# Kernel optimization log

Hardware: AMD Instinct MI355X
Metric: run time of the kernel (lower is better)

Reference implementation:

```python
import jax, jax.numpy as jnp
import numpy as np

T = 5            # Newton-Schulz iterations
NORM_GROUPS = 16 # groups along out_channels
EPS = 1e-5


def setup_inputs() -> dict:
    key = jax.random.key(0)
    # conv weight: [out_ch, in_ch, kh, kw]
    weight = jax.random.normal(key, (2048, 1024, 3, 3), dtype=jnp.float32) * 0.05
    return {"weight": weight}


def reference(weight):
    g = NORM_GROUPS
    out_ch = weight.shape[0]
    Z = weight.reshape(g, out_ch // g, -1)                 # [g, n, d]
    Zc = Z - Z.mean(axis=-1, keepdims=True)                # center each row
    S = jnp.einsum('gnd,gmd->gnm', Zc, Zc)                 # [g, n, n] covariance
    n = S.shape[-1]
    eye = jnp.eye(n, dtype=S.dtype)
    S = S + EPS * eye
    norm_S = jnp.sqrt(jnp.sum(S * S, axis=(1, 2), keepdims=True))  # fro norm, [g,1,1]
    S = S / norm_S

    B0 = jnp.broadcast_to(eye, S.shape)                    # B[0] = I

    def body(B, _):
        B3 = B @ B @ B                                     # matrix_power3
        Bn = 1.5 * B - 0.5 * (B3 @ S)                      # baddbmm(1.5, B, -0.5, B^3, S)
        return Bn, None

    Bt, _ = jax.lax.scan(body, B0, None, length=T)
    W = (Bt @ Zc) / jnp.sqrt(norm_S)                       # [g, n, d]
    return W.reshape(weight.shape)
```

## Files before the change

### kernel.cpp

```cpp
#include <hip/hip_runtime.h>


#define G 16
#define NROW 128
#define D 9216
#define OC 2048
#define KSPLIT 32
#define KCHUNK 288
#define EPSV 1e-5f

typedef float f32x16 __attribute__((ext_vector_type(16)));
typedef __bf16 bf16x8 __attribute__((ext_vector_type(8)));

union Frag {
    uint4 q;
    unsigned short s[8];
    bf16x8 v;
};

static __device__ __forceinline__ unsigned short f2bf(float x) {
    union { float f; unsigned int u; } a; a.f = x;
    unsigned int u = a.u;
    unsigned int r = u + 0x7FFFu + ((u >> 16) & 1u);
    return (unsigned short)(r >> 16);
}

static __device__ __forceinline__ float bf2f(unsigned short s) {
    union { unsigned int u; float f; } a; a.u = ((unsigned int)s) << 16;
    return a.f;
}

static __device__ __forceinline__ int swz(int r, int c) {
    return (r << 7) + ((((c >> 3) ^ (r & 15)) << 3) | (c & 7));
}

__global__ __launch_bounds__(256) void k_sgemm(const float* __restrict__ W,
                                               unsigned short* __restrict__ Zraw,
                                               float* __restrict__ Spart,
                                               float* __restrict__ rowsumPart) {
    __shared__ unsigned short tile[NROW * 128];
    __shared__ float rsum[NROW];
    int bid = blockIdx.x;
    int g = bid >> 5, ks = bid & 31;
    int t = threadIdx.x, lane = t & 63, wave = t >> 6;
    int mq = (wave & 1) * 64, nq = (wave >> 1) * 64;
    int m = lane & 31, h = lane >> 5;

    if (t < 128) rsum[t] = 0.f;

    f32x16 acc[2][2];
#pragma unroll
    for (int i = 0; i < 2; i++)
#pragma unroll
        for (int j = 0; j < 2; j++)
#pragma unroll
            for (int z = 0; z < 16; z++) acc[i][j][z] = 0.f;

    float rs[16], rq[4];
#pragma unroll
    for (int i = 0; i < 16; i++) rs[i] = 0.f;
#pragma unroll
    for (int i = 0; i < 4; i++) rq[i] = 0.f;

    const float* wg = W + (size_t)g * NROW * D + ks * KCHUNK;
    unsigned short* zo = Zraw + (size_t)g * NROW * D + ks * KCHUNK;

    float4 pf[16];
#pragma unroll
    for (int p = 0; p < 16; p++) {
        int fl = p * 256 + t, r = fl >> 5, cf = fl & 31;
        pf[p] = *(const float4*)(wg + (size_t)r * D + cf * 4);
    }

    for (int step = 0; step < 3; step++) {
        __syncthreads();
        if (step < 2) {
            int dbase = step * 128;
#pragma unroll
            for (int p = 0; p < 16; p++) {
                int fl = p * 256 + t, r = fl >> 5, cf = fl & 31;
                float4 x = pf[p];
                rs[p] += x.x + x.y + x.z + x.w;
                ushort4 pk;
                pk.x = f2bf(x.x); pk.y = f2bf(x.y);
                pk.z = f2bf(x.z); pk.w = f2bf(x.w);
                *(ushort4*)(zo + (size_t)r * D + dbase + cf * 4) = pk;
                union { ushort4 s4; uint2 u; } cv; cv.s4 = pk;
                *(uint2*)(tile + swz(r, cf * 4)) = cv.u;
            }
        } else {
#pragma unroll
            for (int p = 0; p < 4; p++) {
                int fl = p * 256 + t, r = fl >> 3, cf = fl & 7;
                float4 x = pf[p];
                rq[p] += x.x + x.y + x.z + x.w;
                ushort4 pk;
                pk.x = f2bf(x.x); pk.y = f2bf(x.y);
                pk.z = f2bf(x.z); pk.w = f2bf(x.w);
                *(ushort4*)(zo + (size_t)r * D + 256 + cf * 4) = pk;
                union { ushort4 s4; uint2 u; } cv; cv.s4 = pk;
                *(uint2*)(tile + swz(r, cf * 4)) = cv.u;
            }
        }
        __syncthreads();
        if (step == 0) {
#pragma unroll
            for (int p = 0; p < 16; p++) {
                int fl = p * 256 + t, r = fl >> 5, cf = fl & 31;
                pf[p] = *(const float4*)(wg + (size_t)r * D + 128 + cf * 4);
            }
        } else if (step == 1) {
#pragma unroll
            for (int p = 0; p < 4; p++) {
                int fl = p * 256 + t, r = fl >> 3, cf = fl & 7;
                pf[p] = *(const float4*)(wg + (size_t)r * D + 256 + cf * 4);
            }
        }
        int kmax = (step < 2) ? 8 : 2;
#pragma unroll
        for (int kk = 0; kk < 8; kk++) {
            if (kk >= kmax) break;
            int kb = kk * 16 + h * 8;
            Frag a0, a1, b0, b1;
            a0.q = *(const uint4*)(tile + swz(mq + m, kb));
            a1.q = *(const uint4*)(tile + swz(mq + 32 + m, kb));
            b0.q = *(const uint4*)(tile + swz(nq + m, kb));
            b1.q = *(const uint4*)(tile + swz(nq + 32 + m, kb));
            acc[0][0] = __builtin_amdgcn_mfma_f32_32x32x16_bf16(a0.v, b0.v, acc[0][0], 0, 0, 0);
            acc[0][1] = __builtin_amdgcn_mfma_f32_32x32x16_bf16(a0.v, b1.v, acc[0][1], 0, 0, 0);
            acc[1][0] = __builtin_amdgcn_mfma_f32_32x32x16_bf16(a1.v, b0.v, acc[1][0], 0, 0, 0);
            acc[1][1] = __builtin_amdgcn_mfma_f32_32x32x16_bf16(a1.v, b1.v, acc[1][1], 0, 0, 0);
        }
    }
    float* sp = Spart + (size_t)bid * 16384;
#pragma unroll
    for (int i = 0; i < 2; i++)
#pragma unroll
        for (int j = 0; j < 2; j++)
#pragma unroll
            for (int reg = 0; reg < 16; reg++) {
                int row = (reg & 3) + 8 * (reg >> 2) + 4 * h;
                sp[(mq + i * 32 + row) * 128 + nq + j * 32 + m] = acc[i][j][reg];
            }
#pragma unroll
    for (int p = 0; p < 16; p++) atomicAdd(&rsum[p * 8 + (t >> 5)], rs[p]);
#pragma unroll
    for (int p = 0; p < 4; p++) atomicAdd(&rsum[p * 32 + (t >> 3)], rq[p]);
    __syncthreads();
    if (t < 128) rowsumPart[bid * 128 + t] = rsum[t];
}

__global__ __launch_bounds__(256) void k_reduce(const float* __restrict__ Spart,
                                                const float* __restrict__ rowsumPart,
                                                float* __restrict__ Sred,
                                                float* __restrict__ normPart) {
    __shared__ float muv[128];
    __shared__ float ls[4];
    int b = blockIdx.x;
    int g = b >> 4, part = b & 15;
    int t = threadIdx.x;
    if (t < 128) {
        float s = 0.f;
        for (int ks = 0; ks < KSPLIT; ks++) s += rowsumPart[(g * KSPLIT + ks) * 128 + t];
        muv[t] = s * (1.0f / 9216.0f);
    }
    __syncthreads();
    int el = part * 1024 + t * 4;
    float4 s = {0.f, 0.f, 0.f, 0.f};
    for (int ks = 0; ks < KSPLIT; ks++) {
        float4 p = *(const float4*)(Spart + (size_t)(g * KSPLIT + ks) * 16384 + el);
        s.x += p.x; s.y += p.y; s.z += p.z; s.w += p.w;
    }
    int r = el >> 7, c = el & 127;
    float4 mc = *(float4*)&muv[c];
    float dm = 9216.0f * muv[r];
    s.x -= dm * mc.x; s.y -= dm * mc.y; s.z -= dm * mc.z; s.w -= dm * mc.w;
    if (r >= c && r <= c + 3) {
        if (r == c) s.x += EPSV;
        else if (r == c + 1) s.y += EPSV;
        else if (r == c + 2) s.z += EPSV;
        else s.w += EPSV;
    }
    *(float4*)(Sred + (size_t)g * 16384 + el) = s;
    float sq = s.x * s.x + s.y * s.y + s.z * s.z + s.w * s.w;
#pragma unroll
    for (int o = 32; o > 0; o >>= 1) sq += __shfl_down(sq, o, 64);
    if ((t & 63) == 0) ls[t >> 6] = sq;
    __syncthreads();
    if (t == 0) normPart[b] = ls[0] + ls[1] + ls[2] + ls[3];
}

__global__ __launch_bounds__(512) void k_ns(const float* __restrict__ Sred,
                                            const float* __restrict__ normPart,
                                            const float* __restrict__ rowsumPart,
                                            unsigned short* __restrict__ Bt,
                                            float* __restrict__ cvec) {
    extern __shared__ unsigned short sm[];
    unsigned short* Bb = sm;
    unsigned short* Sb = sm + 16384;
    unsigned short* Ub = sm + 32768;
    unsigned short* Vt = sm + 49152;
    int g = blockIdx.x;
    int t = threadIdx.x, lane = t & 63, wave = t >> 6;
    int m = lane & 31, h = lane >> 5;

    float ns = 0.f;
#pragma unroll
    for (int i = 0; i < 16; i++) ns += normPart[g * 16 + i];
    float rn = 1.0f / sqrtf(ns);

    {
        int r = t >> 2, c0 = (t & 3) * 32;
        const float* sp = Sred + (size_t)g * 16384 + r * 128 + c0;
#pragma unroll
        for (int q = 0; q < 4; q++) {
            int c = c0 + q * 8;
            float4 x0 = *(const float4*)(sp + q * 8);
            float4 x1 = *(const float4*)(sp + q * 8 + 4);
            float vv[8] = {x0.x, x0.y, x0.z, x0.w, x1.x, x1.y, x1.z, x1.w};
            Frag fs, fb;
#pragma unroll
            for (int i = 0; i < 8; i++) {
                float sv = vv[i] * rn;
                fs.s[i] = f2bf(sv);
                float bv = -0.5f * sv + ((r == c + i) ? 1.5f : 0.f);
                fb.s[i] = f2bf(bv);
            }
            *(uint4*)(Sb + swz(r, c)) = fs.q;
            *(uint4*)(Bb + swz(r, c)) = fb.q;
        }
    }
    Frag fI[2];
#pragma unroll
    for (int kk2 = 0; kk2 < 2; kk2++)
#pragma unroll
        for (int j = 0; j < 8; j++)
            fI[kk2].s[j] = (m == kk2 * 16 + h * 8 + j) ? (unsigned short)0x3FC0
                                                       : (unsigned short)0;
    __syncthreads();

    for (int iter = 0; iter < 4; iter++) {
#pragma unroll
        for (int i = 0; i < 4; i++) {
            int task = wave * 4 + i;
            int tmb = ((task >> 2) & 3) * 32, tnb = (task & 3) * 32;
            const unsigned short* Bsrc = (task < 16) ? Bb : Sb;
            unsigned short* dst = (task < 16) ? Ub : Vt;
            float sc = (task < 16) ? 1.0f : -0.5f;
            f32x16 acc;
#pragma unroll
            for (int z = 0; z < 16; z++) acc[z] = 0.f;
#pragma unroll
            for (int kk = 0; kk < 8; kk++) {
                Frag a, bfr;
                a.q = *(const uint4*)(Bb + swz(tmb + m, kk * 16 + h * 8));
                bfr.q = *(const uint4*)(Bsrc + swz(tnb + m, kk * 16 + h * 8));
                acc = __builtin_amdgcn_mfma_f32_32x32x16_bf16(a.v, bfr.v, acc, 0, 0, 0);
            }
#pragma unroll
            for (int q = 0; q < 4; q++) {
                union { unsigned short s[4]; uint2 u; } pk;
#pragma unroll
                for (int j = 0; j < 4; j++) pk.s[j] = f2bf(sc * acc[q * 4 + j]);
                *(uint2*)(dst + swz(tnb + m, tmb + q * 8 + h * 4)) = pk.u;
            }
        }
        __syncthreads();
        f32x16 acc2[2];
#pragma unroll
        for (int i = 0; i < 2; i++) {
            int task = wave * 2 + i;
            int tmb = (task >> 2) * 32, tnb = (task & 3) * 32;
#pragma unroll
            for (int z = 0; z < 16; z++) acc2[i][z] = 0.f;
#pragma unroll
            for (int kk = 0; kk < 8; kk++) {
                Frag a, bfr;
                a.q = *(const uint4*)(Ub + swz(tmb + m, kk * 16 + h * 8));
                bfr.q = *(const uint4*)(Vt + swz(tnb + m, kk * 16 + h * 8));
                acc2[i] = __builtin_amdgcn_mfma_f32_32x32x16_bf16(a.v, bfr.v, acc2[i], 0, 0, 0);
            }
#pragma unroll
            for (int kk2 = 0; kk2 < 2; kk2++) {
                Frag bfr;
                bfr.q = *(const uint4*)(Bb + swz(tnb + m, tmb + kk2 * 16 + h * 8));
                acc2[i] = __builtin_amdgcn_mfma_f32_32x32x16_bf16(fI[kk2].v, bfr.v, acc2[i], 0, 0, 0);
            }
        }
        __syncthreads();
#pragma unroll
        for (int i = 0; i < 2; i++) {
            int task = wave * 2 + i;
            int tmb = (task >> 2) * 32, tnb = (task & 3) * 32;
#pragma unroll
            for (int q = 0; q < 4; q++) {
                union { unsigned short s[4]; uint2 u; } pk;
#pragma unroll
                for (int j = 0; j < 4; j++) pk.s[j] = f2bf(acc2[i][q * 4 + j]);
                *(uint2*)(Bb + swz(tnb + m, tmb + q * 8 + h * 4)) = pk.u;
            }
        }
        __syncthreads();
    }
    {
        int r = t >> 2, c0 = (t & 3) * 32;
        unsigned short* bp = Bt + (size_t)g * 16384 + r * 128;
#pragma unroll
        for (int q = 0; q < 4; q++) {
            uint4 dd = *(const uint4*)(Bb + swz(r, c0 + q * 8));
            *(uint4*)(bp + c0 + q * 8) = dd;
        }
    }
    float* muv = (float*)(sm + 32768);
    if (t < 128) {
        float s = 0.f;
        for (int ks = 0; ks < KSPLIT; ks++) s += rowsumPart[(g * KSPLIT + ks) * 128 + t];
        muv[t] = s * (1.0f / 9216.0f);
    }
    __syncthreads();
    if (t < 128) {
        float cacc = 0.f;
        for (int k = 0; k < 128; k++) cacc += bf2f(Bb[swz(t, k)]) * muv[k];
        cvec[g * 128 + t] = cacc;
    }
}

__global__ __launch_bounds__(256) void k_wgemm(const unsigned short* __restrict__ Zraw,
                                               const unsigned short* __restrict__ Bt,
                                               const float* __restrict__ normPart,
                                               const float* __restrict__ cvec,
                                               float* __restrict__ out) {
    __shared__ unsigned short Ab[16384];
    __shared__ unsigned short Zt[16384];
    __shared__ float cs[128];
    int nt = blockIdx.x, g = blockIdx.y;
    int t = threadIdx.x, lane = t & 63, wave = t >> 6;
    int m = lane & 31, h = lane >> 5;

    float nsum = 0.f;
#pragma unroll
    for (int i = 0; i < 16; i++) nsum += normPart[g * 16 + i];
    float ss = 1.0f / sqrtf(sqrtf(nsum));

    const unsigned short* bg = Bt + (size_t)g * 16384;
    const unsigned short* zg = Zraw + (size_t)g * NROW * D + nt * 128;
#pragma unroll
    for (int p = 0; p < 8; p++) {
        int flat = p * 256 + t;
        int r = flat >> 4, gc = flat & 15;
        uint4 da = *(const uint4*)(bg + r * 128 + gc * 8);
        uint4 dz = *(const uint4*)(zg + (size_t)r * D + gc * 8);
        *(uint4*)(Ab + swz(r, gc * 8)) = da;
        *(uint4*)(Zt + swz(r, gc * 8)) = dz;
    }
    if (t < 128) cs[t] = cvec[g * 128 + t] * ss;
    __syncthreads();

    int cw = wave * 32 + m;

    f32x16 acc[4];
#pragma unroll
    for (int i = 0; i < 4; i++)
#pragma unroll
        for (int z = 0; z < 16; z++) acc[i][z] = 0.f;

#pragma unroll
    for (int ks = 0; ks < 8; ks++) {
        int k0 = ks * 16 + h * 8;
        Frag b;
#pragma unroll
        for (int j = 0; j < 8; j++) b.s[j] = Zt[swz(k0 + j, cw)];
#pragma unroll
        for (int i = 0; i < 4; i++) {
            Frag a;
            a.q = *(const uint4*)(Ab + swz(i * 32 + m, k0));
            acc[i] = __builtin_amdgcn_mfma_f32_32x32x16_bf16(a.v, b.v, acc[i], 0, 0, 0);
        }
    }
    float* og = out + (size_t)(g * NROW) * D + nt * 128 + cw;
#pragma unroll
    for (int i = 0; i < 4; i++)
#pragma unroll
        for (int reg = 0; reg < 16; reg++) {
            int row = i * 32 + (reg & 3) + 8 * (reg >> 2) + 4 * h;
            og[(size_t)row * D] = acc[i][reg] * ss - cs[row];
        }
}

extern "C" void kernel_launch(void* const* d_in, const int* in_sizes, int n_in,
                              void* d_out, int out_size, void* d_ws, size_t ws_size,
                              hipStream_t stream) {
    const float* W = (const float*)d_in[0];
    float* out = (float*)d_out;
    char* ws = (char*)d_ws;

    unsigned short* Zraw = (unsigned short*)(ws);
    float* Sred = (float*)(ws + 37748736ULL);
    float* normPart = (float*)(ws + 38797312ULL);
    unsigned short* Bt = (unsigned short*)(ws + 38798336ULL);
    float* rowsumPart = (float*)(ws + 39322624ULL);
    float* cvec = (float*)(ws + 39584768ULL);
    float* Spart = out;

    k_sgemm<<<G * KSPLIT, 256, 0, stream>>>(W, Zraw, Spart, rowsumPart);
    k_reduce<<<256, 256, 0, stream>>>(Spart, rowsumPart, Sred, normPart);
    hipFuncSetAttribute((const void*)k_ns,
                        hipFuncAttributeMaxDynamicSharedMemorySize, 131072);
    k_ns<<<G, 512, 131072, stream>>>(Sred, normPart, rowsumPart, Bt, cvec);
    k_wgemm<<<dim3(72, G), 256, 0, stream>>>(Zraw, Bt, normPart, cvec, out);
}
```

Before: 199.4 us.

## Split fp32-to-bf16 conversion and row sums into a separate kernel

Moves the weight conversion to bf16 and the per-row sum into a new per-row kernel, so the covariance GEMM loads pre-converted bf16 tiles directly. This removes conversion work, LDS atomics and register pressure from the GEMM kernel, and the partial row-sum reductions in later kernels. The cost is an extra kernel launch and re-reading the bf16 copy from memory, where previously it was produced on the fly.

```diff
diff --git a/kernel.cpp b/kernel.cpp
--- a/kernel.cpp
+++ b/kernel.cpp
@@ -34,20 +34,41 @@
     return (r << 7) + ((((c >> 3) ^ (r & 15)) << 3) | (c & 7));
 }
 
-__global__ __launch_bounds__(256) void k_sgemm(const float* __restrict__ W,
-                                               unsigned short* __restrict__ Zraw,
-                                               float* __restrict__ Spart,
-                                               float* __restrict__ rowsumPart) {
+__global__ __launch_bounds__(256) void k_convert(const float* __restrict__ W,
+                                                 unsigned short* __restrict__ Zraw,
+                                                 float* __restrict__ rowsum) {
+    __shared__ float ws4[4];
+    int r = blockIdx.x;
+    int t = threadIdx.x;
+    const float* src = W + (size_t)r * D;
+    unsigned short* dst = Zraw + (size_t)r * D;
+    float s = 0.f;
+#pragma unroll
+    for (int it = 0; it < 9; it++) {
+        int idx = it * 1024 + t * 4;
+        float4 x = *(const float4*)(src + idx);
+        s += x.x + x.y + x.z + x.w;
+        ushort4 pk;
+        pk.x = f2bf(x.x); pk.y = f2bf(x.y);
+        pk.z = f2bf(x.z); pk.w = f2bf(x.w);
+        *(ushort4*)(dst + idx) = pk;
+    }
+#pragma unroll
+    for (int o = 32; o > 0; o >>= 1) s += __shfl_down(s, o, 64);
+    if ((t & 63) == 0) ws4[t >> 6] = s;
+    __syncthreads();
+    if (t == 0) rowsum[r] = ws4[0] + ws4[1] + ws4[2] + ws4[3];
+}
+
+__global__ __launch_bounds__(256) void k_sgemm(const unsigned short* __restrict__ Zraw,
+                                               float* __restrict__ Spart) {
     __shared__ unsigned short tile[NROW * 128];
-    __shared__ float rsum[NROW];
     int bid = blockIdx.x;
     int g = bid >> 5, ks = bid & 31;
     int t = threadIdx.x, lane = t & 63, wave = t >> 6;
     int mq = (wave & 1) * 64, nq = (wave >> 1) * 64;
     int m = lane & 31, h = lane >> 5;
 
-    if (t < 128) rsum[t] = 0.f;
-
     f32x16 acc[2][2];
 #pragma unroll
     for (int i = 0; i < 2; i++)
@@ -56,64 +77,42 @@
 #pragma unroll
             for (int z = 0; z < 16; z++) acc[i][j][z] = 0.f;
 
-    float rs[16], rq[4];
-#pragma unroll
-    for (int i = 0; i < 16; i++) rs[i] = 0.f;
-#pragma unroll
-    for (int i = 0; i < 4; i++) rq[i] = 0.f;
-
-    const float* wg = W + (size_t)g * NROW * D + ks * KCHUNK;
-    unsigned short* zo = Zraw + (size_t)g * NROW * D + ks * KCHUNK;
-
-    float4 pf[16];
-#pragma unroll
-    for (int p = 0; p < 16; p++) {
-        int fl = p * 256 + t, r = fl >> 5, cf = fl & 31;
-        pf[p] = *(const float4*)(wg + (size_t)r * D + cf * 4);
+    const unsigned short* zg = Zraw + (size_t)g * NROW * D + ks * KCHUNK;
+
+    uint4 pf[8];
+#pragma unroll
+    for (int p = 0; p < 8; p++) {
+        int fl = p * 256 + t, r = fl >> 4, c8 = (fl & 15) * 8;
+        pf[p] = *(const uint4*)(zg + (size_t)r * D + c8);
     }
 
     for (int step = 0; step < 3; step++) {
         __syncthreads();
         if (step < 2) {
-            int dbase = step * 128;
-#pragma unroll
-            for (int p = 0; p < 16; p++) {
-                int fl = p * 256 + t, r = fl >> 5, cf = fl & 31;
-                float4 x = pf[p];
-                rs[p] += x.x + x.y + x.z + x.w;
-                ushort4 pk;
-                pk.x = f2bf(x.x); pk.y = f2bf(x.y);
-                pk.z = f2bf(x.z); pk.w = f2bf(x.w);
-                *(ushort4*)(zo + (size_t)r * D + dbase + cf * 4) = pk;
-                union { ushort4 s4; uint2 u; } cv; cv.s4 = pk;
-                *(uint2*)(tile + swz(r, cf * 4)) = cv.u;
+#pragma unroll
+            for (int p = 0; p < 8; p++) {
+                int fl = p * 256 + t, r = fl >> 4, c8 = (fl & 15) * 8;
+                *(uint4*)(tile + swz(r, c8)) = pf[p];
             }
         } else {
 #pragma unroll
-            for (int p = 0; p < 4; p++) {
-                int fl = p * 256 + t, r = fl >> 3, cf = fl & 7;
-                float4 x = pf[p];
-                rq[p] += x.x + x.y + x.z + x.w;
-                ushort4 pk;
-                pk.x = f2bf(x.x); pk.y = f2bf(x.y);
-                pk.z = f2bf(x.z); pk.w = f2bf(x.w);
-                *(ushort4*)(zo + (size_t)r * D + 256 + cf * 4) = pk;
-                union { ushort4 s4; uint2 u; } cv; cv.s4 = pk;
-                *(uint2*)(tile + swz(r, cf * 4)) = cv.u;
+            for (int p = 0; p < 2; p++) {
+                int fl = p * 256 + t, r = fl >> 2, c8 = (fl & 3) * 8;
+                *(uint4*)(tile + swz(r, c8)) = pf[p];
             }
         }
         __syncthreads();
         if (step == 0) {
 #pragma unroll
-            for (int p = 0; p < 16; p++) {
-                int fl = p * 256 + t, r = fl >> 5, cf = fl & 31;
-                pf[p] = *(const float4*)(wg + (size_t)r * D + 128 + cf * 4);
+            for (int p = 0; p < 8; p++) {
+                int fl = p * 256 + t, r = fl >> 4, c8 = (fl & 15) * 8;
+                pf[p] = *(const uint4*)(zg + (size_t)r * D + 128 + c8);
             }
         } else if (step == 1) {
 #pragma unroll
-            for (int p = 0; p < 4; p++) {
-                int fl = p * 256 + t, r = fl >> 3, cf = fl & 7;
-                pf[p] = *(const float4*)(wg + (size_t)r * D + 256 + cf * 4);
+            for (int p = 0; p < 2; p++) {
+                int fl = p * 256 + t, r = fl >> 2, c8 = (fl & 3) * 8;
+                pf[p] = *(const uint4*)(zg + (size_t)r * D + 256 + c8);
             }
         }
         int kmax = (step < 2) ? 8 : 2;
@@ -142,16 +141,10 @@
                 int row = (reg & 3) + 8 * (reg >> 2) + 4 * h;
                 sp[(mq + i * 32 + row) * 128 + nq + j * 32 + m] = acc[i][j][reg];
             }
-#pragma unroll
-    for (int p = 0; p < 16; p++) atomicAdd(&rsum[p * 8 + (t >> 5)], rs[p]);
-#pragma unroll
-    for (int p = 0; p < 4; p++) atomicAdd(&rsum[p * 32 + (t >> 3)], rq[p]);
-    __syncthreads();
-    if (t < 128) rowsumPart[bid * 128 + t] = rsum[t];
 }
 
 __global__ __launch_bounds__(256) void k_reduce(const float* __restrict__ Spart,
-                                                const float* __restrict__ rowsumPart,
+                                                const float* __restrict__ rowsum,
                                                 float* __restrict__ Sred,
                                                 float* __restrict__ normPart) {
     __shared__ float muv[128];
@@ -159,11 +152,7 @@
     int b = blockIdx.x;
     int g = b >> 4, part = b & 15;
     int t = threadIdx.x;
-    if (t < 128) {
-        float s = 0.f;
-        for (int ks = 0; ks < KSPLIT; ks++) s += rowsumPart[(g * KSPLIT + ks) * 128 + t];
-        muv[t] = s * (1.0f / 9216.0f);
-    }
+    if (t < 128) muv[t] = rowsum[g * 128 + t] * (1.0f / 9216.0f);
     __syncthreads();
     int el = part * 1024 + t * 4;
     float4 s = {0.f, 0.f, 0.f, 0.f};
@@ -192,7 +181,7 @@
 
 __global__ __launch_bounds__(512) void k_ns(const float* __restrict__ Sred,
                                             const float* __restrict__ normPart,
-                                            const float* __restrict__ rowsumPart,
+                                            const float* __restrict__ rowsum,
                                             unsigned short* __restrict__ Bt,
                                             float* __restrict__ cvec) {
     extern __shared__ unsigned short sm[];
@@ -312,11 +301,7 @@
         }
     }
     float* muv = (float*)(sm + 32768);
-    if (t < 128) {
-        float s = 0.f;
-        for (int ks = 0; ks < KSPLIT; ks++) s += rowsumPart[(g * KSPLIT + ks) * 128 + t];
-        muv[t] = s * (1.0f / 9216.0f);
-    }
+    if (t < 128) muv[t] = rowsum[g * 128 + t] * (1.0f / 9216.0f);
     __syncthreads();
     if (t < 128) {
         float cacc = 0.f;
@@ -398,14 +383,15 @@
     float* Sred = (float*)(ws + 37748736ULL);
     float* normPart = (float*)(ws + 38797312ULL);
     unsigned short* Bt = (unsigned short*)(ws + 38798336ULL);
-    float* rowsumPart = (float*)(ws + 39322624ULL);
-    float* cvec = (float*)(ws + 39584768ULL);
+    float* rowsum = (float*)(ws + 39322624ULL);
+    float* cvec = (float*)(ws + 39330816ULL);
     float* Spart = out;
 
-    k_sgemm<<<G * KSPLIT, 256, 0, stream>>>(W, Zraw, Spart, rowsumPart);
-    k_reduce<<<256, 256, 0, stream>>>(Spart, rowsumPart, Sred, normPart);
+    k_convert<<<OC, 256, 0, stream>>>(W, Zraw, rowsum);
+    k_sgemm<<<G * KSPLIT, 256, 0, stream>>>(Zraw, Spart);
+    k_reduce<<<256, 256, 0, stream>>>(Spart, rowsum, Sred, normPart);
     hipFuncSetAttribute((const void*)k_ns,
                         hipFuncAttributeMaxDynamicSharedMemorySize, 131072);
-    k_ns<<<G, 512, 131072, stream>>>(Sred, normPart, rowsumPart, Bt, cvec);
+    k_ns<<<G, 512, 131072, stream>>>(Sred, normPart, rowsum, Bt, cvec);
     k_wgemm<<<dim3(72, G), 256, 0, stream>>>(Zraw, Bt, normPart, cvec, out);
 }
```

New measurement: 203.0 us. About the same (+1.8%).
